# Performance work log

Hardware: AMD Instinct MI355X
Metric: run time of the kernel (lower is better)

Reference implementation:

```python
import jax, jax.numpy as jnp
from jax import lax
import numpy as np

FILTER_SIZE = 3
PAD = FILTER_SIZE // 2


def _smooth(off, filt):
    # ReflectionPad2d(pad) -> conv2d(padding=pad) -> crop pad:-pad  == same-size smoothing
    x = jnp.pad(off, ((0, 0), (0, 0), (PAD, PAD), (PAD, PAD)), mode='reflect')
    y = lax.conv_general_dilated(x, filt, window_strides=(1, 1),
                                 padding=[(PAD, PAD), (PAD, PAD)],
                                 dimension_numbers=('NCHW', 'OIHW', 'NCHW'))
    return y[:, :, PAD:-PAD, PAD:-PAD]


def _grid_sample(img, gx, gy):
    # img: [C,H,W]; gx,gy: [N,H,W] normalized to [-1,1].
    # Bilinear, align_corners=True, zero padding (torch 1.x default at repo time).
    C, H, W = img.shape
    ix = (gx + 1.0) * 0.5 * (W - 1)
    iy = (gy + 1.0) * 0.5 * (H - 1)
    x0 = jnp.floor(ix); y0 = jnp.floor(iy)
    x1 = x0 + 1.0;      y1 = y0 + 1.0
    wx1 = ix - x0; wx0 = 1.0 - wx1
    wy1 = iy - y0; wy0 = 1.0 - wy1

    def gather(xi, yi):
        valid = ((xi >= 0) & (xi <= W - 1) & (yi >= 0) & (yi <= H - 1)).astype(img.dtype)
        xc = jnp.clip(xi, 0, W - 1).astype(jnp.int32)
        yc = jnp.clip(yi, 0, H - 1).astype(jnp.int32)
        return img[:, yc, xc] * valid[None]  # [C,N,H,W]

    out = (gather(x0, y0) * (wx0 * wy0)[None] +
           gather(x1, y0) * (wx1 * wy0)[None] +
           gather(x0, y1) * (wx0 * wy1)[None] +
           gather(x1, y1) * (wx1 * wy1)[None])
    return out  # [C,N,H,W]


def setup_inputs() -> dict:
    key = jax.random.key(0)
    k1, k2, k3 = jax.random.split(key, 3)
    C, H, W = 16, 512, 960
    F2 = FILTER_SIZE * FILTER_SIZE
    right_input = jax.random.normal(k1, (1, C, H, W), jnp.float32)
    offset_x = jax.random.uniform(k2, (1, 1, H, W), jnp.float32) * 64.0  # disparity-like
    offset_y = jax.random.uniform(k3, (1, 1, H, W), jnp.float32) * 8.0
    x_coordinate = jnp.tile(jnp.arange(W, dtype=jnp.float32)[None, None, None, :], (1, 1, H, 1))
    y_coordinate = jnp.tile(jnp.arange(H, dtype=jnp.float32)[None, None, :, None], (1, 1, 1, W))
    # one-hot neighbour extraction filters: channel i picks neighbour i of the 3x3 patch
    neighbour_extraction_filter = jnp.eye(F2, dtype=jnp.float32).reshape(F2, 1, FILTER_SIZE, FILTER_SIZE)
    return {'right_input': right_input, 'offset_x': offset_x, 'offset_y': offset_y,
            'x_coordinate': x_coordinate, 'y_coordinate': y_coordinate,
            'neighbour_extraction_filter': neighbour_extraction_filter}


def reference(right_input, offset_x, offset_y, x_coordinate, y_coordinate, neighbour_extraction_filter):
    H, W = offset_x.shape[2], offset_x.shape[3]
    sx = _smooth(offset_x, neighbour_extraction_filter)  # [1,F2,H,W]
    sy = _smooth(offset_y, neighbour_extraction_filter)  # [1,F2,H,W]
    coord_x = jnp.clip(x_coordinate - sx, 0.0, W - 1)
    coord_y = jnp.clip(y_coordinate - sy, 0.0, H - 1)
    half_w = W / 2.0; half_h = H / 2.0
    gx = (coord_x - half_w) / half_w  # [1,F2,H,W]
    gy = (coord_y - half_h) / half_h
    # grid batch = 1*F2; instead of repeating right_input F2 times, gather from the
    # single image for all F2 grids at once, then patch-vote (mean over F2).
    rec = _grid_sample(right_input[0], gx[0], gy[0])  # [C,F2,H,W]
    return jnp.mean(rec, axis=1)[None]  # [1,C,H,W]
```

## Files before the change

### kernel.cpp

```cpp
#include <hip/hip_runtime.h>
#include <hip/hip_fp16.h>

#define CH 16
#define HH 512
#define WW 960
#define HW (HH * WW)

#define TR 8
#define TC 64
#define RROWS 18
#define RCOLS 136
#define NSLOT (RROWS * RCOLS)

typedef __fp16 v2hf __attribute__((ext_vector_type(2)));
typedef _Float16 h2r __attribute__((ext_vector_type(2)));

__device__ __forceinline__ unsigned pkrtz_u(float a, float b) {
  v2hf r = __builtin_amdgcn_cvt_pkrtz(a, b);
  return __builtin_bit_cast(unsigned, r);
}
__device__ __forceinline__ __half2 u2h(unsigned u) {
  return __builtin_bit_cast(__half2, u);
}

#define LBAR() asm volatile("s_waitcnt lgkmcnt(0)\n\ts_barrier" ::: "memory")

__global__ __launch_bounds__(512, 6) void recon_fused_f16(
    const float* __restrict__ img,
    const float* __restrict__ offx,
    const float* __restrict__ offy,
    float* __restrict__ out) {
  __shared__ uint4 lds[NSLOT];

  const int hwid = blockIdx.x + blockIdx.y * 15;
  const int tile = (hwid & 7) * 120 + (hwid >> 3);
  const int tx = tile % 15, ty = tile / 15;
  const int x0b = tx * TC, y0b = ty * TR;
  const int tid = threadIdx.x;
  const int ylo = y0b - 9, xlo = x0b - 68;

  const int pixl = tid & 63;
  const int rowl = tid >> 6;
  const int x = x0b + pixl;
  const int y = y0b + rowl;
  const int po = y * WW + x;

  const float fxs = (float)(WW - 1) / (float)WW;
  const float fys = (float)(HH - 1) / (float)HH;
  const float s = 1.0f / 9.0f;

  int u00a[9];
  __half2 wxa[9];
  __half2 wya[9];
#pragma unroll
  for (int di = -1; di <= 1; ++di) {
    int rr = y + di;
    rr = (rr < 0) ? 1 : ((rr >= HH) ? (HH - 2) : rr);
#pragma unroll
    for (int dj = -1; dj <= 1; ++dj) {
      const int n = (di + 1) * 3 + (dj + 1);
      int cc = x + dj;
      cc = (cc < 0) ? 1 : ((cc >= WW) ? (WW - 2) : cc);
      const int o = rr * WW + cc;
      const float sx = offx[o];
      const float sy = offy[o];
      const float cx = fminf(fmaxf((float)x - sx, 0.0f), (float)(WW - 1));
      const float cy = fminf(fmaxf((float)y - sy, 0.0f), (float)(HH - 1));
      const float ix = cx * fxs;
      const float iy = cy * fys;
      const float fx0 = floorf(ix);
      const float fy0 = floorf(iy);
      const float wx1 = ix - fx0, wx0 = 1.0f - wx1;
      const float wy1 = iy - fy0, wy0 = 1.0f - wy1;
      u00a[n] = ((int)fy0 - ylo) * RCOLS + ((int)fx0 - xlo);
      wxa[n] = u2h(pkrtz_u(wx0 * wy0, wx1 * wy0));
      wya[n] = u2h(pkrtz_u(wx0 * wy1, wx1 * wy1));
    }
  }

#pragma unroll
  for (int it = 0; it < 5; ++it) {
    const int f = it * 512 + tid;
    if (f < NSLOT) {
      const int row = f / RCOLS;
      const int col = f - row * RCOLS;
      const int gr = min(max(ylo + row, 0), HH - 1);
      const int gc = min(max(xlo + col, 0), WW - 1);
      const float* src = img + gr * WW + gc;
      uint4 o;
      o.x = pkrtz_u(src[0 * HW], src[1 * HW]);
      o.y = pkrtz_u(src[2 * HW], src[3 * HW]);
      o.z = pkrtz_u(src[4 * HW], src[5 * HW]);
      o.w = pkrtz_u(src[6 * HW], src[7 * HW]);
      lds[f] = o;
    }
  }

  uint4 p1[5];
#pragma unroll
  for (int it = 0; it < 5; ++it) {
    const int f = it * 512 + tid;
    if (f < NSLOT) {
      const int row = f / RCOLS;
      const int col = f - row * RCOLS;
      const int gr = min(max(ylo + row, 0), HH - 1);
      const int gc = min(max(xlo + col, 0), WW - 1);
      const float* src = img + 8 * HW + gr * WW + gc;
      p1[it].x = pkrtz_u(src[0 * HW], src[1 * HW]);
      p1[it].y = pkrtz_u(src[2 * HW], src[3 * HW]);
      p1[it].z = pkrtz_u(src[4 * HW], src[5 * HW]);
      p1[it].w = pkrtz_u(src[6 * HW], src[7 * HW]);
    }
  }

  auto gather_store = [&](int cbase) {
    float acc[8];
#pragma unroll
    for (int i = 0; i < 8; ++i) acc[i] = 0.f;
#pragma unroll
    for (int g = 0; g < 3; ++g) {
      __half2 h[4];
#pragma unroll
      for (int i = 0; i < 4; ++i) h[i] = u2h(0u);
#pragma unroll
      for (int dj = 0; dj < 3; ++dj) {
        const int n = g * 3 + dj;
        const int u00 = u00a[n];
        const __half2 w00 = __half2half2(__low2half(wxa[n]));
        const __half2 w10 = __half2half2(__high2half(wxa[n]));
        const __half2 w01 = __half2half2(__low2half(wya[n]));
        const __half2 w11 = __half2half2(__high2half(wya[n]));
#define CORNER(UIDX, Wh)                          \
  {                                               \
    const uint4 q = lds[(UIDX)];                  \
    h[0] = __hfma2(u2h(q.x), (Wh), h[0]);         \
    h[1] = __hfma2(u2h(q.y), (Wh), h[1]);         \
    h[2] = __hfma2(u2h(q.z), (Wh), h[2]);         \
    h[3] = __hfma2(u2h(q.w), (Wh), h[3]);         \
  }
        CORNER(u00, w00)
        CORNER(u00 + 1, w10)
        CORNER(u00 + RCOLS, w01)
        CORNER(u00 + RCOLS + 1, w11)
#undef CORNER
      }
#pragma unroll
      for (int i = 0; i < 4; ++i) {
        const h2r a = __builtin_bit_cast(h2r, h[i]);
        acc[2 * i]     += (float)a.x;
        acc[2 * i + 1] += (float)a.y;
      }
    }
#pragma unroll
    for (int j = 0; j < 8; ++j) out[(cbase + j) * HW + po] = acc[j] * s;
  };

  LBAR();
  gather_store(0);
  LBAR();

#pragma unroll
  for (int it = 0; it < 5; ++it) {
    const int f = it * 512 + tid;
    if (f < NSLOT) lds[f] = p1[it];
  }
  LBAR();
  gather_store(8);
}

extern "C" void kernel_launch(void* const* d_in, const int* in_sizes, int n_in,
                              void* d_out, int out_size, void* d_ws, size_t ws_size,
                              hipStream_t stream) {
  const float* right = (const float*)d_in[0];
  const float* offx  = (const float*)d_in[1];
  const float* offy  = (const float*)d_in[2];
  float* out = (float*)d_out;

  const dim3 grid(WW / TC, HH / TR);
  recon_fused_f16<<<grid, 512, 0, stream>>>(right, offx, offy, out);
}
```

Baseline: 117.7 us.

## Double-buffer LDS and defer second-half channel packing past first gather

The shared-memory tile is split into two buffers so the second group of 8 channels can be written without a barrier after the first gather. The second half's global loads are now kept as raw floats and only packed to fp16 after the first gather, which lets the load latency overlap with that compute; a sched_barrier keeps that order. Tile source coordinates are computed once and reused, and the occupancy hint drops from 6 to 4 blocks per CU. This doubles LDS use (about 78 KB per block) and holds 40 float registers live, which may reduce occupancy.

```diff
diff --git a/kernel.cpp b/kernel.cpp
--- a/kernel.cpp
+++ b/kernel.cpp
@@ -25,12 +25,12 @@
 
 #define LBAR() asm volatile("s_waitcnt lgkmcnt(0)\n\ts_barrier" ::: "memory")
 
-__global__ __launch_bounds__(512, 6) void recon_fused_f16(
+__global__ __launch_bounds__(512, 4) void recon_fused_f16(
     const float* __restrict__ img,
     const float* __restrict__ offx,
     const float* __restrict__ offy,
     float* __restrict__ out) {
-  __shared__ uint4 lds[NSLOT];
+  __shared__ uint4 lds[2][NSLOT];
 
   const int hwid = blockIdx.x + blockIdx.y * 15;
   const int tile = (hwid & 7) * 120 + (hwid >> 3);
@@ -78,42 +78,40 @@
     }
   }
 
+  int sgr[5], sgc[5];
+#pragma unroll
+  for (int it = 0; it < 5; ++it) {
+    const int f = it * 512 + tid;
+    const int fc = (f < NSLOT) ? f : (NSLOT - 1);
+    const int row = fc / RCOLS;
+    const int col = fc - row * RCOLS;
+    sgr[it] = min(max(ylo + row, 0), HH - 1);
+    sgc[it] = min(max(xlo + col, 0), WW - 1);
+  }
+
 #pragma unroll
   for (int it = 0; it < 5; ++it) {
     const int f = it * 512 + tid;
     if (f < NSLOT) {
-      const int row = f / RCOLS;
-      const int col = f - row * RCOLS;
-      const int gr = min(max(ylo + row, 0), HH - 1);
-      const int gc = min(max(xlo + col, 0), WW - 1);
-      const float* src = img + gr * WW + gc;
+      const float* src = img + sgr[it] * WW + sgc[it];
       uint4 o;
       o.x = pkrtz_u(src[0 * HW], src[1 * HW]);
       o.y = pkrtz_u(src[2 * HW], src[3 * HW]);
       o.z = pkrtz_u(src[4 * HW], src[5 * HW]);
       o.w = pkrtz_u(src[6 * HW], src[7 * HW]);
-      lds[f] = o;
+      lds[0][f] = o;
     }
   }
 
-  uint4 p1[5];
+  float r1[5][8];
 #pragma unroll
   for (int it = 0; it < 5; ++it) {
-    const int f = it * 512 + tid;
-    if (f < NSLOT) {
-      const int row = f / RCOLS;
-      const int col = f - row * RCOLS;
-      const int gr = min(max(ylo + row, 0), HH - 1);
-      const int gc = min(max(xlo + col, 0), WW - 1);
-      const float* src = img + 8 * HW + gr * WW + gc;
-      p1[it].x = pkrtz_u(src[0 * HW], src[1 * HW]);
-      p1[it].y = pkrtz_u(src[2 * HW], src[3 * HW]);
-      p1[it].z = pkrtz_u(src[4 * HW], src[5 * HW]);
-      p1[it].w = pkrtz_u(src[6 * HW], src[7 * HW]);
-    }
+    const float* src = img + 8 * HW + sgr[it] * WW + sgc[it];
+#pragma unroll
+    for (int k = 0; k < 8; ++k) r1[it][k] = src[k * HW];
   }
 
-  auto gather_store = [&](int cbase) {
+  auto gather_store = [&](int buf, int cbase) {
     float acc[8];
 #pragma unroll
     for (int i = 0; i < 8; ++i) acc[i] = 0.f;
@@ -132,7 +130,7 @@
         const __half2 w11 = __half2half2(__high2half(wya[n]));
 #define CORNER(UIDX, Wh)                          \
   {                                               \
-    const uint4 q = lds[(UIDX)];                  \
+    const uint4 q = lds[buf][(UIDX)];             \
     h[0] = __hfma2(u2h(q.x), (Wh), h[0]);         \
     h[1] = __hfma2(u2h(q.y), (Wh), h[1]);         \
     h[2] = __hfma2(u2h(q.z), (Wh), h[2]);         \
@@ -156,16 +154,25 @@
   };
 
   LBAR();
-  gather_store(0);
-  LBAR();
+  gather_store(0, 0);
+
+  __builtin_amdgcn_sched_barrier(0);
 
 #pragma unroll
   for (int it = 0; it < 5; ++it) {
     const int f = it * 512 + tid;
-    if (f < NSLOT) lds[f] = p1[it];
+    if (f < NSLOT) {
+      uint4 o;
+      o.x = pkrtz_u(r1[it][0], r1[it][1]);
+      o.y = pkrtz_u(r1[it][2], r1[it][3]);
+      o.z = pkrtz_u(r1[it][4], r1[it][5]);
+      o.w = pkrtz_u(r1[it][6], r1[it][7]);
+      lds[1][f] = o;
+    }
   }
+
   LBAR();
-  gather_store(8);
+  gather_store(1, 8);
 }
 
 extern "C" void kernel_launch(void* const* d_in, const int* in_sizes, int n_in,
```

Result: faster. 110.9 us (-5.8%).
